# Kernel optimization log

Measured on AMD Instinct MI355X. Metric: run time of the kernel, lower is better.

Reference implementation:

```python
import jax, jax.numpy as jnp
import numpy as np

H = 512
TEMPERATURE = 1.0


def setup_inputs() -> dict:
    key = jax.random.key(0)
    ks = jax.random.split(key, 9)
    B, Q, S = 4, 64, 1024
    scale = 1.0 / np.sqrt(H)
    return {
        "query": jax.random.normal(ks[0], (B, Q, H), jnp.float32),
        "key_": jax.random.normal(ks[1], (B, S, H), jnp.float32),
        "value": jax.random.normal(ks[2], (B, S, H), jnp.float32),
        "Wq": jax.random.normal(ks[3], (H, H), jnp.float32) * scale,
        "bq": jax.random.normal(ks[4], (H,), jnp.float32) * 0.01,
        "Wk": jax.random.normal(ks[5], (H, H), jnp.float32) * scale,
        "bk": jax.random.normal(ks[6], (H,), jnp.float32) * 0.01,
        "we": jax.random.normal(ks[7], (H,), jnp.float32) * scale,
        "be": jax.random.normal(ks[8], (), jnp.float32) * 0.01,
    }


def reference(query, key_, value, Wq, bq, Wk, bk, we, be):
    # query: [B,Q,H], key_/value: [B,S,H]
    qp = jnp.einsum("bqd,dh->bqh", query, Wq) + bq          # [B,Q,H]
    kp = jnp.einsum("bsd,dh->bsh", key_, Wk) + bk           # [B,S,H]
    attn_sum = jnp.tanh(qp[:, :, None, :] + kp[:, None, :, :])  # [B,Q,S,H]
    scores = (jnp.einsum("bqsh,h->bqs", attn_sum, we) + be) / TEMPERATURE
    weights = jax.nn.softmax(scores, axis=-1)               # [B,Q,S]
    context = jnp.einsum("bqs,bsh->bqh", weights, value)    # [B,Q,H]
    return context, weights
```

## Files before the change

### kernel.cpp

```cpp
#include <hip/hip_runtime.h>


constexpr int kB = 4;
constexpr int kQ = 64;
constexpr int kS = 1024;
constexpr int kH = 512;

typedef short bf16x8 __attribute__((ext_vector_type(8)));
typedef float f32x4 __attribute__((ext_vector_type(4)));

__device__ __forceinline__ unsigned bf16rtn_bits(float x) {
  unsigned u = __float_as_uint(x);
  u += 0x7FFFu + ((u >> 16) & 1u);
  return u;
}

__global__ __launch_bounds__(256) void convert_w(
    const float* __restrict__ Wk, const float* __restrict__ Wq,
    unsigned short* __restrict__ Bhi, unsigned short* __restrict__ Blo) {
  const int gid = blockIdx.x * 256 + threadIdx.x;
  const int c = gid & 63;
  const int g = (gid >> 6) & 3;
  const int kt = (gid >> 8) & 15;
  const int ct = (gid >> 12) & 7;
  const int mat = gid >> 15;
  const float* W = mat ? Wq : Wk;
  const float* src = W + (size_t)(kt * 32 + g * 8) * kH + ct * 64 + c;
  bf16x8 hv, lv;
#pragma unroll
  for (int j = 0; j < 8; j++) {
    float x = src[(size_t)j * kH];
    unsigned u = bf16rtn_bits(x);
    float hf = __uint_as_float(u & 0xFFFF0000u);
    unsigned v = bf16rtn_bits(x - hf);
    hv[j] = (short)(u >> 16);
    lv[j] = (short)(v >> 16);
  }
  *(bf16x8*)(Bhi + (size_t)gid * 8) = hv;
  *(bf16x8*)(Blo + (size_t)gid * 8) = lv;
}

__global__ __launch_bounds__(256) void convert_x(
    const float* __restrict__ key_, const float* __restrict__ query,
    unsigned short* __restrict__ Xhi, unsigned short* __restrict__ Xlo) {
  __shared__ __align__(16) unsigned short LHi[128 * 40];
  __shared__ __align__(16) unsigned short LLo[128 * 40];
  const int kt = blockIdx.x;
  const int rt = blockIdx.y;
  const float* X = (rt < 32) ? (key_ + (size_t)rt * 128 * kH)
                             : (query + (size_t)(rt - 32) * 128 * kH);
  const int t = threadIdx.x;
  const int r = t >> 1, c0 = (t & 1) * 16;
  const float* src = X + (size_t)r * kH + kt * 32 + c0;
  bf16x8 hv0, hv1, lv0, lv1;
#pragma unroll
  for (int i = 0; i < 16; i++) {
    float x = src[i];
    unsigned u = bf16rtn_bits(x);
    float hf = __uint_as_float(u & 0xFFFF0000u);
    unsigned v = bf16rtn_bits(x - hf);
    if (i < 8) { hv0[i] = (short)(u >> 16); lv0[i] = (short)(v >> 16); }
    else       { hv1[i - 8] = (short)(u >> 16); lv1[i - 8] = (short)(v >> 16); }
  }
  *(bf16x8*)&LHi[r * 40 + c0] = hv0;
  *(bf16x8*)&LHi[r * 40 + c0 + 8] = hv1;
  *(bf16x8*)&LLo[r * 40 + c0] = lv0;
  *(bf16x8*)&LLo[r * 40 + c0 + 8] = lv1;
  __syncthreads();
  const size_t obase = (size_t)(rt * 16 + kt) * 512 * 8;
#pragma unroll
  for (int p = 0; p < 2; p++) {
    const int s = t + p * 256;
    const int rr = s & 127, g = s >> 7;
    *(uint4*)(Xhi + obase + (size_t)s * 8) = *(const uint4*)&LHi[rr * 40 + g * 8];
    *(uint4*)(Xlo + obase + (size_t)s * 8) = *(const uint4*)&LLo[rr * 40 + g * 8];
  }
}

__global__ __launch_bounds__(512) void proj_mfma(
    const unsigned short* __restrict__ Xhi, const unsigned short* __restrict__ Xlo,
    const unsigned short* __restrict__ Bhi, const unsigned short* __restrict__ Blo,
    const float* __restrict__ bk, const float* __restrict__ bq,
    float* __restrict__ Ek, float* __restrict__ Eq) {
  __shared__ __align__(16) unsigned short AhiL[2][4096];
  __shared__ __align__(16) unsigned short AloL[2][4096];
  __shared__ __align__(16) unsigned short BhiL[2][2048];
  __shared__ __align__(16) unsigned short BloL[2][2048];

  const int ct = blockIdx.x;
  const int rt = blockIdx.y;
  const int mat = (rt >= 32) ? 1 : 0;
  const float* bias = mat ? bq : bk;
  float* Y = mat ? (Eq + (size_t)(rt - 32) * 128 * kH)
                 : (Ek + (size_t)rt * 128 * kH);

  const int t = threadIdx.x;
  const unsigned short* ah_src = Xhi + ((size_t)(rt * 16) * 512 + t) * 8;
  const unsigned short* al_src = Xlo + ((size_t)(rt * 16) * 512 + t) * 8;
  const int bslot = t & 255;
  const unsigned short* b_src =
      ((t < 256) ? Bhi : Blo) + ((size_t)((mat * 8 + ct) * 16) * 256 + bslot) * 8;

  uint4 pah, pal, pb;
  auto gload = [&](int kt2) {
    pah = *(const uint4*)(ah_src + (size_t)kt2 * 512 * 8);
    pal = *(const uint4*)(al_src + (size_t)kt2 * 512 * 8);
    pb = *(const uint4*)(b_src + (size_t)kt2 * 256 * 8);
  };
  auto lwrite = [&](int buf) {
    *(uint4*)&AhiL[buf][t * 8] = pah;
    *(uint4*)&AloL[buf][t * 8] = pal;
    if (t < 256) *(uint4*)&BhiL[buf][bslot * 8] = pb;
    else         *(uint4*)&BloL[buf][bslot * 8] = pb;
  };

  const int l = t & 63, lg = l >> 4, lr = l & 15;
  const int wv = t >> 6, wm = wv & 3, wn = wv >> 2;

  f32x4 acc[2][2];
#pragma unroll
  for (int m = 0; m < 2; m++)
#pragma unroll
    for (int n = 0; n < 2; n++) acc[m][n] = {0.f, 0.f, 0.f, 0.f};

  gload(0);
  lwrite(0);
  __syncthreads();

  for (int kt2 = 0; kt2 < 16; kt2++) {
    if (kt2 < 15) gload(kt2 + 1);

    const unsigned short* Ah = AhiL[kt2 & 1];
    const unsigned short* Al = AloL[kt2 & 1];
    const unsigned short* Bh = BhiL[kt2 & 1];
    const unsigned short* Bl = BloL[kt2 & 1];
    bf16x8 ah[2], al[2], bh[2], bl[2];
#pragma unroll
    for (int m = 0; m < 2; m++) {
      const int off = (lg * 128 + wm * 32 + m * 16 + lr) * 8;
      ah[m] = *(const bf16x8*)(Ah + off);
      al[m] = *(const bf16x8*)(Al + off);
    }
#pragma unroll
    for (int n = 0; n < 2; n++) {
      const int off = (lg * 64 + wn * 32 + n * 16 + lr) * 8;
      bh[n] = *(const bf16x8*)(Bh + off);
      bl[n] = *(const bf16x8*)(Bl + off);
    }
#pragma unroll
    for (int m = 0; m < 2; m++)
#pragma unroll
      for (int n = 0; n < 2; n++) {
        acc[m][n] = __builtin_amdgcn_mfma_f32_16x16x32_bf16(ah[m], bh[n], acc[m][n], 0, 0, 0);
        acc[m][n] = __builtin_amdgcn_mfma_f32_16x16x32_bf16(al[m], bh[n], acc[m][n], 0, 0, 0);
        acc[m][n] = __builtin_amdgcn_mfma_f32_16x16x32_bf16(ah[m], bl[n], acc[m][n], 0, 0, 0);
      }

    if (kt2 < 15) {
      __syncthreads();
      lwrite((kt2 + 1) & 1);
      __syncthreads();
    }
  }

  const int col0 = ct * 64 + wn * 32 + lr;
  const float b0 = bias[col0];
  const float b1 = bias[col0 + 16];
#pragma unroll
  for (int m = 0; m < 2; m++) {
    const int row0 = wm * 32 + m * 16 + lg * 4;
#pragma unroll
    for (int jj = 0; jj < 4; jj++) {
      float* y = Y + (size_t)(row0 + jj) * kH;
      y[col0]      = __expf(2.f * (acc[m][0][jj] + b0));
      y[col0 + 16] = __expf(2.f * (acc[m][1][jj] + b1));
    }
  }
}

__global__ __launch_bounds__(256) void score_kernel(
    const float* __restrict__ Eq, const float* __restrict__ Ek,
    const float* __restrict__ we, float* __restrict__ sout) {
  __shared__ __align__(16) float EkL[2][64 * 64];

  const int qt = blockIdx.x, st = blockIdx.y, b = blockIdx.z;
  const int t = threadIdx.x, lane = t & 63;
  const int wvu = __builtin_amdgcn_readfirstlane(t >> 6);
  const int s0 = st * 64;
  const int q0g = b * kQ + qt * 8;
  const int qA = wvu * 2;

  const float4* we4 = (const float4*)we;
  {
  }
  float4 u0 = we4[lane * 2], u1 = we4[lane * 2 + 1];
  float wsum = u0.x + u0.y + u0.z + u0.w + u1.x + u1.y + u1.z + u1.w;
#pragma unroll
  for (int off = 32; off; off >>= 1) wsum += __shfl_xor(wsum, off);

  const float4* qa4 = (const float4*)(Eq + (size_t)(q0g + qA) * kH);
  const float4* qb4 = (const float4*)(Eq + (size_t)(q0g + qA + 1) * kH);

  const int er = t >> 4;
  const int ej = t & 15;
  const float* ekg = Ek + (size_t)(b * kS + s0 + er) * kH + ej * 4;
  float4 pk[4];
  auto gload = [&](int c) {
#pragma unroll
    for (int i = 0; i < 4; i++)
      pk[i] = *(const float4*)(ekg + (size_t)(16 * i) * kH + c * 64);
  };
  auto lwrite = [&](int buf) {
#pragma unroll
    for (int i = 0; i < 4; i++) {
      const int row = er + 16 * i;
      *(float4*)(&EkL[buf][row * 64 + ((ej ^ (row & 15)) << 2)]) = pk[i];
    }
  };

  gload(0);
  lwrite(0);
  __syncthreads();

  float accA = 0.f, accB = 0.f;
  const int sw = lane & 15;

  for (int c = 0; c < 8; c++) {
    if (c < 7) gload(c + 1);
    const float* ekb = &EkL[c & 1][lane * 64];
#pragma unroll 4
    for (int g = 0; g < 16; g++) {
      float4 ek = *(const float4*)(ekb + ((g ^ sw) << 2));
      float4 w = we4[c * 16 + g];
      float4 qa = qa4[c * 16 + g];
      float4 qb = qb4[c * 16 + g];
      {
        float a1 = fmaf(qa.x, ek.x, 1.f), b1 = fmaf(qa.y, ek.y, 1.f);
        float n1 = fmaf(w.y, a1, w.x * b1);
        accA = fmaf(n1, __builtin_amdgcn_rcpf(a1 * b1), accA);
        float a2 = fmaf(qa.z, ek.z, 1.f), b2 = fmaf(qa.w, ek.w, 1.f);
        float n2 = fmaf(w.w, a2, w.z * b2);
        accA = fmaf(n2, __builtin_amdgcn_rcpf(a2 * b2), accA);
      }
      {
        float a1 = fmaf(qb.x, ek.x, 1.f), b1 = fmaf(qb.y, ek.y, 1.f);
        float n1 = fmaf(w.y, a1, w.x * b1);
        accB = fmaf(n1, __builtin_amdgcn_rcpf(a1 * b1), accB);
        float a2 = fmaf(qb.z, ek.z, 1.f), b2 = fmaf(qb.w, ek.w, 1.f);
        float n2 = fmaf(w.w, a2, w.z * b2);
        accB = fmaf(n2, __builtin_amdgcn_rcpf(a2 * b2), accB);
      }
    }
    if (c < 7) {
      __syncthreads();
      lwrite((c + 1) & 1);
      __syncthreads();
    }
  }

  sout[(size_t)(q0g + qA + 0) * kS + s0 + lane] = fmaf(-2.f, accA, wsum);
  sout[(size_t)(q0g + qA + 1) * kS + s0 + lane] = fmaf(-2.f, accB, wsum);
}

__global__ __launch_bounds__(256) void softmax_kernel(float* __restrict__ wout) {
  __shared__ float redm[4];
  __shared__ float reds[4];
  const int row = blockIdx.x;
  const int t = threadIdx.x, wave = t >> 6, lane = t & 63;
  float4* rp = (float4*)(wout + (size_t)row * kS);
  float4 v = rp[t];

  float m = fmaxf(fmaxf(v.x, v.y), fmaxf(v.z, v.w));
#pragma unroll
  for (int off = 32; off; off >>= 1) m = fmaxf(m, __shfl_xor(m, off));
  if (lane == 0) redm[wave] = m;
  __syncthreads();
  m = fmaxf(fmaxf(redm[0], redm[1]), fmaxf(redm[2], redm[3]));

  float4 e;
  e.x = __expf(v.x - m); e.y = __expf(v.y - m);
  e.z = __expf(v.z - m); e.w = __expf(v.w - m);
  float sum = e.x + e.y + e.z + e.w;
#pragma unroll
  for (int off = 32; off; off >>= 1) sum += __shfl_xor(sum, off);
  if (lane == 0) reds[wave] = sum;
  __syncthreads();
  sum = reds[0] + reds[1] + reds[2] + reds[3];
  float inv = 1.f / sum;
  e.x *= inv; e.y *= inv; e.z *= inv; e.w *= inv;
  rp[t] = e;
}

__global__ __launch_bounds__(256) void context_kernel(
    const float* __restrict__ wout, const float* __restrict__ value,
    float* __restrict__ part) {
  __shared__ __align__(16) float wt[128][16];
  const int bx = blockIdx.x;
  const int sc = bx & 7, qc = (bx >> 3) & 3, hc = (bx >> 5) & 1, b = bx >> 6;
  const int t = threadIdx.x;
  const int s0 = sc * 128, q0 = qc * 16;

  {
    const int q_l = t & 15;
    const int sseg = (t >> 4) * 8;
    const float4* p4 =
        (const float4*)(wout + (size_t)(b * kQ + q0 + q_l) * kS + s0 + sseg);
    float4 u0 = p4[0], u1 = p4[1];
    wt[sseg + 0][q_l] = u0.x; wt[sseg + 1][q_l] = u0.y;
    wt[sseg + 2][q_l] = u0.z; wt[sseg + 3][q_l] = u0.w;
    wt[sseg + 4][q_l] = u1.x; wt[sseg + 5][q_l] = u1.y;
    wt[sseg + 6][q_l] = u1.z; wt[sseg + 7][q_l] = u1.w;
  }
  __syncthreads();

  const int h = hc * 256 + t;
  const float* vb = value + ((size_t)b * kS + s0) * kH + h;
  float acc[16];
#pragma unroll
  for (int i = 0; i < 16; i++) acc[i] = 0.f;

#pragma unroll 4
  for (int s = 0; s < 128; s++) {
    float v = vb[(size_t)s * kH];
    const float4* wrow = (const float4*)&wt[s][0];
    float4 a0 = wrow[0], a1 = wrow[1], a2 = wrow[2], a3 = wrow[3];
    acc[0]  = fmaf(a0.x, v, acc[0]);  acc[1]  = fmaf(a0.y, v, acc[1]);
    acc[2]  = fmaf(a0.z, v, acc[2]);  acc[3]  = fmaf(a0.w, v, acc[3]);
    acc[4]  = fmaf(a1.x, v, acc[4]);  acc[5]  = fmaf(a1.y, v, acc[5]);
    acc[6]  = fmaf(a1.z, v, acc[6]);  acc[7]  = fmaf(a1.w, v, acc[7]);
    acc[8]  = fmaf(a2.x, v, acc[8]);  acc[9]  = fmaf(a2.y, v, acc[9]);
    acc[10] = fmaf(a2.z, v, acc[10]); acc[11] = fmaf(a2.w, v, acc[11]);
    acc[12] = fmaf(a3.x, v, acc[12]); acc[13] = fmaf(a3.y, v, acc[13]);
    acc[14] = fmaf(a3.z, v, acc[14]); acc[15] = fmaf(a3.w, v, acc[15]);
  }

  float* pp = part + (size_t)sc * kB * kQ * kH;
#pragma unroll
  for (int i = 0; i < 16; i++)
    pp[(size_t)(b * kQ + q0 + i) * kH + h] = acc[i];
}

__global__ __launch_bounds__(256) void reduce_kernel(
    const float* __restrict__ part, float* __restrict__ ctx) {
  const int i = blockIdx.x * 256 + threadIdx.x;
  float4 a = {0, 0, 0, 0};
#pragma unroll
  for (int p = 0; p < 8; p++) {
    float4 v = ((const float4*)(part + (size_t)p * kB * kQ * kH))[i];
    a.x += v.x; a.y += v.y; a.z += v.z; a.w += v.w;
  }
  ((float4*)ctx)[i] = a;
}

extern "C" void kernel_launch(void* const* d_in, const int* in_sizes, int n_in,
                              void* d_out, int out_size, void* d_ws,
                              size_t ws_size, hipStream_t stream) {
  const float* query = (const float*)d_in[0];
  const float* key_  = (const float*)d_in[1];
  const float* value = (const float*)d_in[2];
  const float* Wq    = (const float*)d_in[3];
  const float* bq    = (const float*)d_in[4];
  const float* Wk    = (const float*)d_in[5];
  const float* bk    = (const float*)d_in[6];
  const float* we    = (const float*)d_in[7];

  float* ctx  = (float*)d_out;
  float* wout = (float*)d_out + (size_t)kB * kQ * kH;

  float* Eq   = (float*)d_ws;
  float* Ek   = Eq + (size_t)kB * kQ * kH;
  float* part = Ek;
  unsigned short* Bhi =
      (unsigned short*)((char*)d_ws + (size_t)(kB * kQ * kH + kB * kS * kH) * 4);
  unsigned short* Blo = Bhi + (size_t)2 * 8 * 16 * 256 * 8;
  unsigned short* Xhi = Blo + (size_t)2 * 8 * 16 * 256 * 8;
  unsigned short* Xlo = Xhi + (size_t)34 * 16 * 512 * 8;

  convert_w<<<256, 256, 0, stream>>>(Wk, Wq, Bhi, Blo);
  convert_x<<<dim3(16, 34), 256, 0, stream>>>(key_, query, Xhi, Xlo);
  proj_mfma<<<dim3(8, 34), 512, 0, stream>>>(Xhi, Xlo, Bhi, Blo, bk, bq, Ek, Eq);
  score_kernel<<<dim3(8, 16, 4), 256, 0, stream>>>(Eq, Ek, we, wout);
  softmax_kernel<<<kB * kQ, 256, 0, stream>>>(wout);
  context_kernel<<<256, 256, 0, stream>>>(wout, value, part);
  reduce_kernel<<<kB * kQ * kH / 4 / 256, 256, 0, stream>>>(part, ctx);
}
```

Before: 154.4 us.

## Fuse softmax, context and reduction into one kernel; merge conversion kernels

After: 148.4 us. 1.04x faster.

```diff
diff --git a/kernel.cpp b/kernel.cpp
--- a/kernel.cpp
+++ b/kernel.cpp
@@ -15,41 +15,43 @@
   return u;
 }
 
-__global__ __launch_bounds__(256) void convert_w(
+__global__ __launch_bounds__(256) void convert_all(
     const float* __restrict__ Wk, const float* __restrict__ Wq,
-    unsigned short* __restrict__ Bhi, unsigned short* __restrict__ Blo) {
-  const int gid = blockIdx.x * 256 + threadIdx.x;
-  const int c = gid & 63;
-  const int g = (gid >> 6) & 3;
-  const int kt = (gid >> 8) & 15;
-  const int ct = (gid >> 12) & 7;
-  const int mat = gid >> 15;
-  const float* W = mat ? Wq : Wk;
-  const float* src = W + (size_t)(kt * 32 + g * 8) * kH + ct * 64 + c;
-  bf16x8 hv, lv;
-#pragma unroll
-  for (int j = 0; j < 8; j++) {
-    float x = src[(size_t)j * kH];
-    unsigned u = bf16rtn_bits(x);
-    float hf = __uint_as_float(u & 0xFFFF0000u);
-    unsigned v = bf16rtn_bits(x - hf);
-    hv[j] = (short)(u >> 16);
-    lv[j] = (short)(v >> 16);
-  }
-  *(bf16x8*)(Bhi + (size_t)gid * 8) = hv;
-  *(bf16x8*)(Blo + (size_t)gid * 8) = lv;
-}
-
-__global__ __launch_bounds__(256) void convert_x(
     const float* __restrict__ key_, const float* __restrict__ query,
+    unsigned short* __restrict__ Bhi, unsigned short* __restrict__ Blo,
     unsigned short* __restrict__ Xhi, unsigned short* __restrict__ Xlo) {
   __shared__ __align__(16) unsigned short LHi[128 * 40];
   __shared__ __align__(16) unsigned short LLo[128 * 40];
-  const int kt = blockIdx.x;
-  const int rt = blockIdx.y;
+  const int bid = blockIdx.x;
+  const int t = threadIdx.x;
+  if (bid < 256) {
+    const int gid = bid * 256 + t;
+    const int c = gid & 63;
+    const int g = (gid >> 6) & 3;
+    const int kt = (gid >> 8) & 15;
+    const int ct = (gid >> 12) & 7;
+    const int mat = gid >> 15;
+    const float* W = mat ? Wq : Wk;
+    const float* src = W + (size_t)(kt * 32 + g * 8) * kH + ct * 64 + c;
+    bf16x8 hv, lv;
+#pragma unroll
+    for (int j = 0; j < 8; j++) {
+      float x = src[(size_t)j * kH];
+      unsigned u = bf16rtn_bits(x);
+      float hf = __uint_as_float(u & 0xFFFF0000u);
+      unsigned v = bf16rtn_bits(x - hf);
+      hv[j] = (short)(u >> 16);
+      lv[j] = (short)(v >> 16);
+    }
+    *(bf16x8*)(Bhi + (size_t)gid * 8) = hv;
+    *(bf16x8*)(Blo + (size_t)gid * 8) = lv;
+    return;
+  }
+  const int xb = bid - 256;
+  const int kt = xb & 15;
+  const int rt = xb >> 4;
   const float* X = (rt < 32) ? (key_ + (size_t)rt * 128 * kH)
                              : (query + (size_t)(rt - 32) * 128 * kH);
-  const int t = threadIdx.x;
   const int r = t >> 1, c0 = (t & 1) * 16;
   const float* src = X + (size_t)r * kH + kt * 32 + c0;
   bf16x8 hv0, hv1, lv0, lv1;
@@ -180,7 +182,7 @@
 
 __global__ __launch_bounds__(256) void score_kernel(
     const float* __restrict__ Eq, const float* __restrict__ Ek,
-    const float* __restrict__ we, float* __restrict__ sout) {
+    const float* __restrict__ we, float* __restrict__ sraw) {
   __shared__ __align__(16) float EkL[2][64 * 64];
 
   const int qt = blockIdx.x, st = blockIdx.y, b = blockIdx.z;
@@ -191,8 +193,6 @@
   const int qA = wvu * 2;
 
   const float4* we4 = (const float4*)we;
-  {
-  }
   float4 u0 = we4[lane * 2], u1 = we4[lane * 2 + 1];
   float wsum = u0.x + u0.y + u0.z + u0.w + u1.x + u1.y + u1.z + u1.w;
 #pragma unroll
@@ -258,98 +258,87 @@
     }
   }
 
-  sout[(size_t)(q0g + qA + 0) * kS + s0 + lane] = fmaf(-2.f, accA, wsum);
-  sout[(size_t)(q0g + qA + 1) * kS + s0 + lane] = fmaf(-2.f, accB, wsum);
-}
-
-__global__ __launch_bounds__(256) void softmax_kernel(float* __restrict__ wout) {
-  __shared__ float redm[4];
-  __shared__ float reds[4];
-  const int row = blockIdx.x;
-  const int t = threadIdx.x, wave = t >> 6, lane = t & 63;
-  float4* rp = (float4*)(wout + (size_t)row * kS);
-  float4 v = rp[t];
-
-  float m = fmaxf(fmaxf(v.x, v.y), fmaxf(v.z, v.w));
+  sraw[(size_t)(q0g + qA + 0) * kS + s0 + lane] = fmaf(-2.f, accA, wsum);
+  sraw[(size_t)(q0g + qA + 1) * kS + s0 + lane] = fmaf(-2.f, accB, wsum);
+}
+
+__global__ __launch_bounds__(256) void ctx_fused(
+    const float* __restrict__ sraw, const float* __restrict__ value,
+    float* __restrict__ wout, float* __restrict__ ctx) {
+  __shared__ __align__(16) float wt[4][1024];
+  __shared__ __align__(16) float parts[4][4][128];
+  const int bid = blockIdx.x;
+  const int qc = bid >> 4, b = (bid >> 2) & 3, hc = bid & 3;
+  const int t = threadIdx.x, wv = t >> 6, lane = t & 63;
+  const int grow = b * kQ + qc * 4 + wv;
+
+  const float4* row4 = (const float4*)(sraw + (size_t)grow * kS);
+  float4 v[4];
+#pragma unroll
+  for (int j = 0; j < 4; j++) v[j] = row4[lane + 64 * j];
+  float m = -1e30f;
+#pragma unroll
+  for (int j = 0; j < 4; j++)
+    m = fmaxf(m, fmaxf(fmaxf(v[j].x, v[j].y), fmaxf(v[j].z, v[j].w)));
 #pragma unroll
   for (int off = 32; off; off >>= 1) m = fmaxf(m, __shfl_xor(m, off));
-  if (lane == 0) redm[wave] = m;
-  __syncthreads();
-  m = fmaxf(fmaxf(redm[0], redm[1]), fmaxf(redm[2], redm[3]));
-
-  float4 e;
-  e.x = __expf(v.x - m); e.y = __expf(v.y - m);
-  e.z = __expf(v.z - m); e.w = __expf(v.w - m);
-  float sum = e.x + e.y + e.z + e.w;
+  float sum = 0.f;
+#pragma unroll
+  for (int j = 0; j < 4; j++) {
+    v[j].x = __expf(v[j].x - m); v[j].y = __expf(v[j].y - m);
+    v[j].z = __expf(v[j].z - m); v[j].w = __expf(v[j].w - m);
+    sum += v[j].x + v[j].y + v[j].z + v[j].w;
+  }
 #pragma unroll
   for (int off = 32; off; off >>= 1) sum += __shfl_xor(sum, off);
-  if (lane == 0) reds[wave] = sum;
-  __syncthreads();
-  sum = reds[0] + reds[1] + reds[2] + reds[3];
-  float inv = 1.f / sum;
-  e.x *= inv; e.y *= inv; e.z *= inv; e.w *= inv;
-  rp[t] = e;
-}
-
-__global__ __launch_bounds__(256) void context_kernel(
-    const float* __restrict__ wout, const float* __restrict__ value,
-    float* __restrict__ part) {
-  __shared__ __align__(16) float wt[128][16];
-  const int bx = blockIdx.x;
-  const int sc = bx & 7, qc = (bx >> 3) & 3, hc = (bx >> 5) & 1, b = bx >> 6;
-  const int t = threadIdx.x;
-  const int s0 = sc * 128, q0 = qc * 16;
-
-  {
-    const int q_l = t & 15;
-    const int sseg = (t >> 4) * 8;
-    const float4* p4 =
-        (const float4*)(wout + (size_t)(b * kQ + q0 + q_l) * kS + s0 + sseg);
-    float4 u0 = p4[0], u1 = p4[1];
-    wt[sseg + 0][q_l] = u0.x; wt[sseg + 1][q_l] = u0.y;
-    wt[sseg + 2][q_l] = u0.z; wt[sseg + 3][q_l] = u0.w;
-    wt[sseg + 4][q_l] = u1.x; wt[sseg + 5][q_l] = u1.y;
-    wt[sseg + 6][q_l] = u1.z; wt[sseg + 7][q_l] = u1.w;
-  }
-  __syncthreads();
-
-  const int h = hc * 256 + t;
-  const float* vb = value + ((size_t)b * kS + s0) * kH + h;
-  float acc[16];
-#pragma unroll
-  for (int i = 0; i < 16; i++) acc[i] = 0.f;
-
-#pragma unroll 4
-  for (int s = 0; s < 128; s++) {
-    float v = vb[(size_t)s * kH];
-    const float4* wrow = (const float4*)&wt[s][0];
-    float4 a0 = wrow[0], a1 = wrow[1], a2 = wrow[2], a3 = wrow[3];
-    acc[0]  = fmaf(a0.x, v, acc[0]);  acc[1]  = fmaf(a0.y, v, acc[1]);
-    acc[2]  = fmaf(a0.z, v, acc[2]);  acc[3]  = fmaf(a0.w, v, acc[3]);
-    acc[4]  = fmaf(a1.x, v, acc[4]);  acc[5]  = fmaf(a1.y, v, acc[5]);
-    acc[6]  = fmaf(a1.z, v, acc[6]);  acc[7]  = fmaf(a1.w, v, acc[7]);
-    acc[8]  = fmaf(a2.x, v, acc[8]);  acc[9]  = fmaf(a2.y, v, acc[9]);
-    acc[10] = fmaf(a2.z, v, acc[10]); acc[11] = fmaf(a2.w, v, acc[11]);
-    acc[12] = fmaf(a3.x, v, acc[12]); acc[13] = fmaf(a3.y, v, acc[13]);
-    acc[14] = fmaf(a3.z, v, acc[14]); acc[15] = fmaf(a3.w, v, acc[15]);
-  }
-
-  float* pp = part + (size_t)sc * kB * kQ * kH;
-#pragma unroll
-  for (int i = 0; i < 16; i++)
-    pp[(size_t)(b * kQ + q0 + i) * kH + h] = acc[i];
-}
-
-__global__ __launch_bounds__(256) void reduce_kernel(
-    const float* __restrict__ part, float* __restrict__ ctx) {
-  const int i = blockIdx.x * 256 + threadIdx.x;
-  float4 a = {0, 0, 0, 0};
-#pragma unroll
-  for (int p = 0; p < 8; p++) {
-    float4 v = ((const float4*)(part + (size_t)p * kB * kQ * kH))[i];
-    a.x += v.x; a.y += v.y; a.z += v.z; a.w += v.w;
-  }
-  ((float4*)ctx)[i] = a;
+  const float inv = 1.f / sum;
+  float4* wrow = (float4*)&wt[wv][0];
+  float4* gw = (float4*)(wout + (size_t)grow * kS);
+#pragma unroll
+  for (int j = 0; j < 4; j++) {
+    v[j].x *= inv; v[j].y *= inv; v[j].z *= inv; v[j].w *= inv;
+    wrow[lane + 64 * j] = v[j];
+    if (hc == 0) gw[lane + 64 * j] = v[j];
+  }
+  __syncthreads();
+
+  const float* vbase =
+      value + ((size_t)b * kS + wv * 256) * kH + hc * 128 + lane * 2;
+  float2 acc[4];
+#pragma unroll
+  for (int q = 0; q < 4; q++) acc[q] = {0.f, 0.f};
+#pragma unroll 2
+  for (int s4 = 0; s4 < 64; s4++) {
+    float4 wq[4];
+#pragma unroll
+    for (int q = 0; q < 4; q++)
+      wq[q] = *(const float4*)&wt[q][wv * 256 + s4 * 4];
+#pragma unroll
+    for (int u = 0; u < 4; u++) {
+      const float2 vv = *(const float2*)(vbase + (size_t)(s4 * 4 + u) * kH);
+      const float w0 = ((const float*)&wq[0])[u];
+      const float w1 = ((const float*)&wq[1])[u];
+      const float w2 = ((const float*)&wq[2])[u];
+      const float w3 = ((const float*)&wq[3])[u];
+      acc[0].x = fmaf(w0, vv.x, acc[0].x); acc[0].y = fmaf(w0, vv.y, acc[0].y);
+      acc[1].x = fmaf(w1, vv.x, acc[1].x); acc[1].y = fmaf(w1, vv.y, acc[1].y);
+      acc[2].x = fmaf(w2, vv.x, acc[2].x); acc[2].y = fmaf(w2, vv.y, acc[2].y);
+      acc[3].x = fmaf(w3, vv.x, acc[3].x); acc[3].y = fmaf(w3, vv.y, acc[3].y);
+    }
+  }
+#pragma unroll
+  for (int q = 0; q < 4; q++)
+    *(float2*)&parts[wv][q][lane * 2] = acc[q];
+  __syncthreads();
+
+  const int q = t >> 6, hp = t & 63;
+  float2 r = {0.f, 0.f};
+#pragma unroll
+  for (int w = 0; w < 4; w++) {
+    const float2 p2 = *(const float2*)&parts[w][q][hp * 2];
+    r.x += p2.x; r.y += p2.y;
+  }
+  *(float2*)(ctx + (size_t)(b * kQ + qc * 4 + q) * kH + hc * 128 + hp * 2) = r;
 }
 
 extern "C" void kernel_launch(void* const* d_in, const int* in_sizes, int n_in,
@@ -367,20 +356,17 @@
   float* ctx  = (float*)d_out;
   float* wout = (float*)d_out + (size_t)kB * kQ * kH;
 
-  float* Eq   = (float*)d_ws;
-  float* Ek   = Eq + (size_t)kB * kQ * kH;
-  float* part = Ek;
+  float* Eq = (float*)d_ws;
+  float* Ek = Eq + (size_t)kB * kQ * kH;
   unsigned short* Bhi =
       (unsigned short*)((char*)d_ws + (size_t)(kB * kQ * kH + kB * kS * kH) * 4);
   unsigned short* Blo = Bhi + (size_t)2 * 8 * 16 * 256 * 8;
   unsigned short* Xhi = Blo + (size_t)2 * 8 * 16 * 256 * 8;
   unsigned short* Xlo = Xhi + (size_t)34 * 16 * 512 * 8;
-
-  convert_w<<<256, 256, 0, stream>>>(Wk, Wq, Bhi, Blo);
-  convert_x<<<dim3(16, 34), 256, 0, stream>>>(key_, query, Xhi, Xlo);
+  float* sraw = (float*)(Xlo + (size_t)34 * 16 * 512 * 8);
+
+  convert_all<<<800, 256, 0, stream>>>(Wk, Wq, key_, query, Bhi, Blo, Xhi, Xlo);
   proj_mfma<<<dim3(8, 34), 512, 0, stream>>>(Xhi, Xlo, Bhi, Blo, bk, bq, Ek, Eq);
-  score_kernel<<<dim3(8, 16, 4), 256, 0, stream>>>(Eq, Ek, we, wout);
-  softmax_kernel<<<kB * kQ, 256, 0, stream>>>(wout);
-  context_kernel<<<256, 256, 0, stream>>>(wout, value, part);
-  reduce_kernel<<<kB * kQ * kH / 4 / 256, 256, 0, stream>>>(part, ctx);
-}
+  score_kernel<<<dim3(8, 16, 4), 256, 0, stream>>>(Eq, Ek, we, sraw);
+  ctx_fused<<<256, 256, 0, stream>>>(sraw, value, wout, ctx);
+}
```
